# Kernel tuning notes

Measured on AMD Instinct MI355X. Metric: run time of the kernel, lower is better.

Reference implementation:

```python
import jax, jax.numpy as jnp
import numpy as np

H, W, P = 480, 600, 2048
N = H * W
_IU = np.triu_indices(4)

def _conv(x, w, b, stride=1):
    y = jax.lax.conv_general_dilated(x, w, (stride, stride), 'SAME',
                                     dimension_numbers=('NCHW', 'OIHW', 'NCHW'))
    return y + b[None, :, None, None]

def _gn(x, scale, bias, groups=16, eps=1e-5):
    n, c, h, w = x.shape
    xg = x.reshape(n, groups, c // groups, h, w)
    mu = xg.mean(axis=(2, 3, 4), keepdims=True)
    var = xg.var(axis=(2, 3, 4), keepdims=True)
    xg = (xg - mu) * jax.lax.rsqrt(var + eps)
    return xg.reshape(n, c, h, w) * scale[None, :, None, None] + bias[None, :, None, None]

def _lrelu(x):
    return jnp.where(x >= 0, x, 0.2 * x)

def setup_inputs():
    key = jax.random.key(0)
    ks = jax.random.split(key, 16)
    def he(k, shape, fan_in):
        return jax.random.normal(k, shape, jnp.float32) * np.float32(np.sqrt(2.0 / fan_in))
    return {
        'depth': jax.random.normal(ks[0], (1, 1, H, W), jnp.float32),
        'pose': jax.random.normal(ks[1], (P, 2, 8), jnp.float32),
        'target_mask': (jax.random.uniform(ks[2], (1, 1, H, W)) > 0.5).astype(jnp.float32),
        'pairs': jax.random.randint(ks[3], (P, 2), 0, N),
        'conv1_w': he(ks[4], (32, 3, 3, 3), 3 * 9), 'conv1_b': jnp.zeros(32),
        'gn1_s': jnp.ones(32), 'gn1_b': jnp.zeros(32),
        'conv2_w': he(ks[5], (64, 32, 3, 3), 32 * 9), 'conv2_b': jnp.zeros(64),
        'gn2_s': jnp.ones(64), 'gn2_b': jnp.zeros(64),
        'conv3_w': he(ks[6], (64, 64, 3, 3), 64 * 9), 'conv3_b': jnp.zeros(64),
        'gn3_s': jnp.ones(64), 'gn3_b': jnp.zeros(64),
        'conv4_w': he(ks[7], (64, 96, 3, 3), 96 * 9), 'conv4_b': jnp.zeros(64),
        'gn4_s': jnp.ones(64), 'gn4_b': jnp.zeros(64),
        'gate_w': he(ks[8], (15, 64), 15), 'gate_b': jnp.zeros(64),
        'hid_w': he(ks[9], (64, 64), 64), 'hid_b': jnp.zeros(64),
        'out_w': he(ks[10], (64, 1), 64), 'out_b': jnp.zeros(1),
    }

def _forward(depth, pose, target_mask, params, pairs):
    (c1w, c1b, g1s, g1b, c2w, c2b, g2s, g2b, c3w, c3b, g3s, g3b,
     c4w, c4b, g4s, g4b, gw, gb, hw_, hb, ow, ob) = params
    idx = pairs[:, 0]
    hh, ww = idx // W, idx % W
    # vectorized replacement of the per-pair python-loop scatter
    attn = jnp.zeros((1, 1, H, W), jnp.float32).at[0, 0, hh, ww].set(1.0)
    std_depth = (depth - depth.mean()) * 10.0
    x = jnp.concatenate([std_depth, target_mask, attn], axis=1)  # [1,3,H,W]
    # res_unet backbone (encoder-decoder, GroupNorm, leaky-relu 0.2)
    c1 = _lrelu(_gn(_conv(x, c1w, c1b), g1s, g1b))               # [1,32,H,W]
    d1 = _lrelu(_gn(_conv(c1, c2w, c2b, stride=2), g2s, g2b))    # [1,64,H/2,W/2]
    bm = _lrelu(_gn(_conv(d1, c3w, c3b), g3s, g3b))              # [1,64,H/2,W/2]
    up = jax.image.resize(bm, (1, 64, H, W), method='nearest')
    u = jnp.concatenate([up, c1], axis=1)                         # [1,96,H,W]
    feats = _lrelu(_gn(_conv(u, c4w, c4b), g4s, g4b))            # [1,64,H,W]
    # vectorized per-pair gather
    fg = feats.reshape(64, N)[:, idx].T                           # [P,64]
    fg = jnp.broadcast_to(fg[:, None, :], (P, 2, 64))
    dg = std_depth.reshape(N)[idx]
    dg = jnp.broadcast_to(dg[:, None, None], (P, 2, 1))
    quat = pose[:, :, :4]
    fingers = pose[:, :, 4:7]
    trans = pose[:, :, 7:8]
    outer = quat[..., :, None] * quat[..., None, :]               # sign-invariant q_i*q_j
    enc = outer[..., _IU[0], _IU[1]]                              # [P,2,10]
    cond = jnp.concatenate([enc, fingers, trans, dg], axis=-1)    # [P,2,15]
    # ContextGate_1d: gated attention over gathered features
    gate = jax.nn.sigmoid(cond @ gw + gb)                         # [P,2,64]
    h = fg * gate
    h = h * jax.lax.rsqrt(jnp.sum(h * h, axis=-1, keepdims=True) + 1e-8)
    h = _lrelu(h @ hw_ + hb)
    return jax.nn.silu(h) @ ow + ob                               # [P,2,1]

def reference(depth, pose, target_mask, pairs, conv1_w, conv1_b, gn1_s, gn1_b,
              conv2_w, conv2_b, gn2_s, gn2_b, conv3_w, conv3_b, gn3_s, gn3_b,
              conv4_w, conv4_b, gn4_s, gn4_b, gate_w, gate_b, hid_w, hid_b,
              out_w, out_b):
    params = (conv1_w, conv1_b, gn1_s, gn1_b, conv2_w, conv2_b, gn2_s, gn2_b,
              conv3_w, conv3_b, gn3_s, gn3_b, conv4_w, conv4_b, gn4_s, gn4_b,
              gate_w, gate_b, hid_w, hid_b, out_w, out_b)
    return _forward(depth, pose, target_mask, params, pairs)
```

## Files before the change

kernel.cpp:

```cpp
#include <hip/hip_runtime.h>
#include <math.h>

#define HH 480
#define WW 600
#define NN (HH*WW)
#define PP 2048
#define H2 240
#define W2 300
#define N2 (H2*W2)

typedef __bf16  bf16x8  __attribute__((ext_vector_type(8)));
typedef float   f32x4   __attribute__((ext_vector_type(4)));
typedef ushort  ushort8 __attribute__((ext_vector_type(8)));

__device__ __forceinline__ ushort f2b(float f) {
    unsigned u = __float_as_uint(f);
    unsigned r = (u + 0x7FFF + ((u >> 16) & 1)) >> 16;
    return (ushort)r;
}

constexpr size_t alup(size_t x) { return (x + 4095) & ~(size_t)4095; }
constexpr size_t OFF_X   = 4096;
constexpr size_t OFF_FT  = alup(OFF_X   + 3UL*NN*4);
constexpr size_t OFF_C1P = alup(OFF_FT  + 64UL*NN*4);
constexpr size_t OFF_D1R = alup(OFF_C1P + 32UL*NN*2);
constexpr size_t OFF_D1P = alup(OFF_D1R + 64UL*N2*4);
constexpr size_t OFF_BMP = alup(OFF_D1P + 64UL*N2*2);
constexpr size_t OFF_WB2 = alup(OFF_BMP + 64UL*N2*2);
constexpr size_t OFF_WB3 = alup(OFF_WB2 + 36864UL);
constexpr size_t OFF_WB4 = alup(OFF_WB3 + 73728UL);

__global__ void k_sum(const float* __restrict__ d, float* __restrict__ ws) {
    float s = 0.f;
    for (int i = blockIdx.x*blockDim.x + threadIdx.x; i < NN; i += gridDim.x*blockDim.x)
        s += d[i];
    #pragma unroll
    for (int o = 32; o; o >>= 1) s += __shfl_down(s, o, 64);
    __shared__ float sm[4];
    int wid = threadIdx.x >> 6;
    if ((threadIdx.x & 63) == 0) sm[wid] = s;
    __syncthreads();
    if (threadIdx.x == 0) {
        float t = 0.f;
        for (int w = 0; w < (int)(blockDim.x >> 6); ++w) t += sm[w];
        atomicAdd(ws, t);
    }
}

__global__ void k_buildx(const float* __restrict__ depth, const float* __restrict__ mask,
                         const float* __restrict__ ws, float* __restrict__ x) {
    int i = blockIdx.x*blockDim.x + threadIdx.x;
    if (i >= NN) return;
    float mean = ws[0] * (1.0f/NN);
    x[i]        = (depth[i] - mean) * 10.0f;
    x[NN + i]   = mask[i];
    x[2*NN + i] = 0.f;
}

__global__ void k_scatter(const int* __restrict__ pairs, float* __restrict__ x) {
    int p = blockIdx.x*blockDim.x + threadIdx.x;
    if (p < PP) x[2*NN + pairs[2*p]] = 1.0f;
}

__global__ void k_wcvt(const float* __restrict__ w, ushort* __restrict__ dst, int NCH) {
    int e = blockIdx.x*256 + threadIdx.x;
    int total = 9*NCH*64*32;
    if (e >= total) return;
    int k  = e & 31;
    int co = (e >> 5) & 63;
    int rest = e >> 11;
    int c = rest % NCH;
    int t = rest / NCH;
    dst[e] = f2b(w[(co*(NCH*32) + c*32 + k)*9 + t]);
}

template<int CIN, int TCO>
__global__ __launch_bounds__(64) void k_conv1(const float* __restrict__ in,
        const float* __restrict__ w, const float* __restrict__ bias,
        float* __restrict__ out) {
    int x   = blockIdx.x*64 + threadIdx.x;
    int y   = blockIdx.y;
    int co0 = blockIdx.z*TCO;
    if (x >= WW) return;
    float acc[TCO];
    #pragma unroll
    for (int c = 0; c < TCO; ++c) acc[c] = bias[co0+c];
    int  xb   = x - 1;
    bool xint = (xb >= 0) && (xb + 2 < WW);
    for (int ci = 0; ci < CIN; ++ci) {
        const float* ip = in + (long)ci*NN;
        float iv[3][3];
        #pragma unroll
        for (int dy = 0; dy < 3; ++dy) {
            int iy = y + dy - 1;
            if ((unsigned)iy < (unsigned)HH) {
                const float* rp = ip + (long)iy*WW + xb;
                if (xint) { iv[dy][0]=rp[0]; iv[dy][1]=rp[1]; iv[dy][2]=rp[2]; }
                else {
                    #pragma unroll
                    for (int dx = 0; dx < 3; ++dx) {
                        int ix = xb + dx;
                        iv[dy][dx] = ((unsigned)ix < (unsigned)WW) ? ip[(long)iy*WW+ix] : 0.f;
                    }
                }
            } else iv[dy][0]=iv[dy][1]=iv[dy][2]=0.f;
        }
        const float* wp = w + ((long)co0*CIN + ci)*9;
        #pragma unroll
        for (int c = 0; c < TCO; ++c)
            #pragma unroll
            for (int k = 0; k < 9; ++k)
                acc[c] += iv[k/3][k%3] * wp[(long)c*CIN*9 + k];
    }
    float* op = out + (size_t)(y*WW + x)*32 + co0;
    #pragma unroll
    for (int c = 0; c < TCO; ++c) op[c] = acc[c];
}

__global__ __launch_bounds__(256) void k_gnstats_pk(const float* __restrict__ x,
        float* __restrict__ stat, int npx) {
    int o = threadIdx.x & 3;
    float s[8], s2[8];
    #pragma unroll
    for (int j = 0; j < 8; ++j) { s[j] = 0.f; s2[j] = 0.f; }
    for (int e = blockIdx.x*256 + threadIdx.x; e < npx*4; e += gridDim.x*256) {
        int px = e >> 2;
        const float* p = x + (size_t)px*32 + o*8;
        #pragma unroll
        for (int j = 0; j < 8; ++j) { float v = p[j]; s[j] += v; s2[j] += v*v; }
    }
    float gs[4], gs2[4];
    #pragma unroll
    for (int j = 0; j < 4; ++j) { gs[j] = s[2*j]+s[2*j+1]; gs2[j] = s2[2*j]+s2[2*j+1]; }
    #pragma unroll
    for (int off = 4; off < 64; off <<= 1)
        #pragma unroll
        for (int j = 0; j < 4; ++j) {
            gs[j]  += __shfl_xor(gs[j],  off, 64);
            gs2[j] += __shfl_xor(gs2[j], off, 64);
        }
    __shared__ float sm[4][4][8];
    int wv = threadIdx.x >> 6;
    if ((threadIdx.x & 63) < 4) {
        #pragma unroll
        for (int j = 0; j < 4; ++j) { sm[wv][o][j] = gs[j]; sm[wv][o][4+j] = gs2[j]; }
    }
    __syncthreads();
    if (threadIdx.x < 32) {
        int o2 = threadIdx.x >> 3, k = threadIdx.x & 7;
        float t = sm[0][o2][k] + sm[1][o2][k] + sm[2][o2][k] + sm[3][o2][k];
        int g = o2*4 + (k & 3);
        atomicAdd(&stat[(k >> 2)*16 + g], t);
    }
}

template<int CH, int CHPER>
__global__ void k_gnpack(const float* __restrict__ x, ushort* __restrict__ y,
                         const float* __restrict__ scale, const float* __restrict__ bias,
                         const float* __restrict__ stat, int npx) {
    constexpr int PARTS = CH/16;
    int e = blockIdx.x*256 + threadIdx.x;
    if (e >= npx*PARTS) return;
    int px   = e / PARTS;
    int part = e - px*PARTS;
    const float* p = x + (size_t)px*CH + part*16;
    ushort*      q = y + (size_t)px*CH + part*16;
    float cnt = (float)CHPER * (float)npx;
    #pragma unroll
    for (int j = 0; j < 16; ++j) {
        int c = part*16 + j;
        int g = c / CHPER;
        float mu  = stat[g] / cnt;
        float var = stat[16+g] / cnt - mu*mu;
        float rs  = rsqrtf(var + 1e-5f);
        float v = (p[j] - mu) * rs * scale[c] + bias[c];
        q[j] = f2b(v >= 0.f ? v : 0.2f*v);
    }
}

template<int MODE>
__global__ __launch_bounds__(256) void k_sconv(const ushort* __restrict__ inA,
        const ushort* __restrict__ inB, const ushort* __restrict__ wb,
        const float* __restrict__ bias, float* __restrict__ out,
        float* __restrict__ stat) {
    constexpr int Wo   = (MODE==4) ? WW : W2;
    constexpr int NCH  = (MODE==2) ? 1 : (MODE==3) ? 2 : 3;
    constexpr int NPT  = (MODE==2) ? 2 : 4;
    constexpr int ROWS = (MODE==2) ? 9 : 6;
    constexpr int PXS  = 68;
    constexpr int CPITCH = 36;
    constexpr int UNITS = ROWS*PXS*4;
    constexpr int Hi = (MODE==3) ? H2 : HH;
    constexpr int Wi = (MODE==3) ? W2 : WW;
    __shared__ __align__(16) ushort sh[ROWS*PXS*CPITCH];
    __shared__ float sred[4][16][2];

    int w    = threadIdx.x >> 6;
    int lane = threadIdx.x & 63;
    int lm   = lane & 15;
    int lg   = lane >> 4;
    int y0   = blockIdx.y*4;
    int x0   = blockIdx.x*(NPT*16);
    int y    = y0 + w;
    int iy0  = (MODE==2) ? 2*y0 : y0 - 1;
    int ix0  = (MODE==2) ? 2*x0 : x0 - 1;

    f32x4 acc[4][NPT];
    #pragma unroll
    for (int ct = 0; ct < 4; ++ct)
        #pragma unroll
        for (int pt = 0; pt < NPT; ++pt) acc[ct][pt] = 0.f;

    int dsbase = (((MODE==2 ? 2*w*PXS + 2*lm : w*PXS + lm))*CPITCH + lg*8);

    #pragma unroll
    for (int kc = 0; kc < NCH; ++kc) {
        if (kc) __syncthreads();
        #pragma unroll
        for (int u0 = 0; u0 < UNITS; u0 += 256) {
            int u = u0 + threadIdx.x;
            if (u < UNITS) {
                int r  = u / (PXS*4);
                int rm = u - r*(PXS*4);
                int px = rm >> 2;
                int q  = rm & 3;
                int iy = iy0 + r;
                int ix = ix0 + px;
                ushort8 val = {};
                if ((unsigned)iy < (unsigned)Hi && (unsigned)ix < (unsigned)Wi) {
                    const ushort* sp;
                    if (MODE==2)      sp = inA + ((size_t)iy*WW + ix)*32 + q*8;
                    else if (MODE==3) sp = inA + ((size_t)iy*W2 + ix)*64 + kc*32 + q*8;
                    else if (kc < 2)  sp = inA + ((size_t)(iy>>1)*W2 + (ix>>1))*64 + kc*32 + q*8;
                    else              sp = inB + ((size_t)iy*WW + ix)*32 + q*8;
                    val = *(const ushort8*)sp;
                }
                *(ushort8*)&sh[(r*PXS + px)*CPITCH + q*8] = val;
            }
        }
        __syncthreads();
        #pragma unroll
        for (int t = 0; t < 9; ++t) {
            const int dy = t/3, dx = t - 3*(t/3);
            const ushort* wp = wb + (size_t)((t*NCH + kc)*64)*32;
            bf16x8 a[4];
            #pragma unroll
            for (int ct = 0; ct < 4; ++ct)
                a[ct] = *(const bf16x8*)(wp + (ct*16 + lm)*32 + lg*8);
            #pragma unroll
            for (int pt = 0; pt < NPT; ++pt) {
                int off = (dy*PXS + (MODE==2 ? pt*32 + dx : pt*16 + dx))*CPITCH;
                bf16x8 b = *(const bf16x8*)&sh[dsbase + off];
                #pragma unroll
                for (int ct = 0; ct < 4; ++ct)
                    acc[ct][pt] = __builtin_amdgcn_mfma_f32_16x16x32_bf16(a[ct], b, acc[ct][pt], 0, 0, 0);
            }
        }
    }

    #pragma unroll
    for (int ct = 0; ct < 4; ++ct) {
        float s = 0.f, s2 = 0.f;
        #pragma unroll
        for (int pt = 0; pt < NPT; ++pt) {
            int pxg = x0 + pt*16 + lm;
            bool vld = pxg < Wo;
            f32x4 r;
            #pragma unroll
            for (int reg = 0; reg < 4; ++reg) {
                int co = ct*16 + lg*4 + reg;
                float v = acc[ct][pt][reg] + bias[co];
                r[reg] = v;
                if (vld) { s += v; s2 += v*v; }
            }
            if (vld)
                *(f32x4*)(out + (size_t)(y*Wo + pxg)*64 + ct*16 + lg*4) = r;
        }
        #pragma unroll
        for (int o = 1; o < 16; o <<= 1) {
            s  += __shfl_xor(s,  o, 64);
            s2 += __shfl_xor(s2, o, 64);
        }
        if (lm == 0) { sred[w][ct*4+lg][0] = s; sred[w][ct*4+lg][1] = s2; }
    }
    __syncthreads();
    if (threadIdx.x < 32) {
        int g = threadIdx.x >> 1, k = threadIdx.x & 1;
        float t = sred[0][g][k] + sred[1][g][k] + sred[2][g][k] + sred[3][g][k];
        atomicAdd(&stat[k*16 + g], t);
    }
}

__global__ void k_mlp(const float* __restrict__ pose, const float* __restrict__ sd,
                      const int* __restrict__ pairs, const float* __restrict__ feats,
                      const float* __restrict__ g4s, const float* __restrict__ g4b,
                      const float* __restrict__ st4,
                      const float* __restrict__ gw, const float* __restrict__ gb,
                      const float* __restrict__ hw, const float* __restrict__ hb,
                      const float* __restrict__ ow, const float* __restrict__ ob,
                      float* __restrict__ out) {
    int wid  = threadIdx.x >> 6;
    int lane = threadIdx.x & 63;
    int t = blockIdx.x*4 + wid;
    int p = t >> 1;
    const float* pp = pose + t*8;
    float q0=pp[0], q1=pp[1], q2=pp[2], q3=pp[3];
    float f0=pp[4], f1=pp[5], f2=pp[6], tr=pp[7];
    int idx = pairs[2*p];
    float dg = sd[idx];
    float cond[15] = {q0*q0,q0*q1,q0*q2,q0*q3,q1*q1,q1*q2,q1*q3,q2*q2,q2*q3,q3*q3,
                      f0,f1,f2,tr,dg};
    float acc = gb[lane];
    #pragma unroll
    for (int k = 0; k < 15; ++k) acc += cond[k]*gw[k*64+lane];
    float gate = 1.f/(1.f+expf(-acc));
    float raw = feats[(size_t)idx*64 + lane];
    int   g4  = lane >> 2;
    float cnt = 4.0f * (float)NN;
    float mu  = st4[g4] / cnt;
    float var = st4[16+g4] / cnt - mu*mu;
    float rs  = rsqrtf(var + 1e-5f);
    float fv  = (raw - mu) * rs * g4s[lane] + g4b[lane];
    float fg  = fv >= 0.f ? fv : 0.2f*fv;
    float h = fg*gate;
    float ss = h*h;
    #pragma unroll
    for (int o = 32; o; o >>= 1) ss += __shfl_xor(ss, o, 64);
    h *= rsqrtf(ss + 1e-8f);
    __shared__ float hs[4][64];
    hs[wid][lane] = h;
    __syncthreads();
    float a2 = hb[lane];
    #pragma unroll 8
    for (int d = 0; d < 64; ++d) a2 += hs[wid][d]*hw[d*64+lane];
    float h2 = a2 >= 0.f ? a2 : 0.2f*a2;
    float si = h2 / (1.f+expf(-h2));
    float v = si * ow[lane];
    #pragma unroll
    for (int o = 32; o; o >>= 1) v += __shfl_xor(v, o, 64);
    if (lane == 0) out[t] = v + ob[0];
}

extern "C" void kernel_launch(void* const* d_in, const int* in_sizes, int n_in,
                              void* d_out, int out_size, void* d_ws, size_t ws_size,
                              hipStream_t stream) {
    const float* depth = (const float*)d_in[0];
    const float* pose  = (const float*)d_in[1];
    const float* mask  = (const float*)d_in[2];
    const int*   pairs = (const int*)  d_in[3];
    const float* c1w = (const float*)d_in[4];  const float* c1b = (const float*)d_in[5];
    const float* g1s = (const float*)d_in[6];  const float* g1b = (const float*)d_in[7];
    const float* c2w = (const float*)d_in[8];  const float* c2b = (const float*)d_in[9];
    const float* g2s = (const float*)d_in[10]; const float* g2b = (const float*)d_in[11];
    const float* c3w = (const float*)d_in[12]; const float* c3b = (const float*)d_in[13];
    const float* g3s = (const float*)d_in[14]; const float* g3b = (const float*)d_in[15];
    const float* c4w = (const float*)d_in[16]; const float* c4b = (const float*)d_in[17];
    const float* g4s = (const float*)d_in[18]; const float* g4b = (const float*)d_in[19];
    const float* gw  = (const float*)d_in[20]; const float* gb  = (const float*)d_in[21];
    const float* hw_ = (const float*)d_in[22]; const float* hb  = (const float*)d_in[23];
    const float* ow  = (const float*)d_in[24]; const float* ob  = (const float*)d_in[25];

    char* base = (char*)d_ws;
    float*  stats = (float*) base;
    float*  X   = (float*) (base + OFF_X);
    float*  FT  = (float*) (base + OFF_FT);
    float*  C1R = FT;
    ushort* C1P = (ushort*)(base + OFF_C1P);
    float*  D1R = (float*) (base + OFF_D1R);
    ushort* D1P = (ushort*)(base + OFF_D1P);
    ushort* BMP = (ushort*)(base + OFF_BMP);
    ushort* WB2 = (ushort*)(base + OFF_WB2);
    ushort* WB3 = (ushort*)(base + OFF_WB3);
    ushort* WB4 = (ushort*)(base + OFF_WB4);
    float* st1 = stats + 16;
    float* st2 = stats + 64;
    float* st3 = stats + 112;
    float* st4 = stats + 160;

    hipMemsetAsync(d_ws, 0, 1024, stream);

    k_sum    <<<1024, 256, 0, stream>>>(depth, stats);
    k_buildx <<<(NN+255)/256, 256, 0, stream>>>(depth, mask, stats, X);
    k_scatter<<<(PP+255)/256, 256, 0, stream>>>(pairs, X);
    k_wcvt   <<< 72, 256, 0, stream>>>(c2w, WB2, 1);
    k_wcvt   <<<144, 256, 0, stream>>>(c3w, WB3, 2);
    k_wcvt   <<<216, 256, 0, stream>>>(c4w, WB4, 3);

    k_conv1<3,16><<<dim3(10, HH, 2), 64, 0, stream>>>(X, c1w, c1b, C1R);
    k_gnstats_pk<<<256, 256, 0, stream>>>(C1R, st1, NN);
    k_gnpack<32,2><<<(NN*2+255)/256, 256, 0, stream>>>(C1R, C1P, g1s, g1b, st1, NN);

    k_sconv<2><<<dim3(10, 60), 256, 0, stream>>>(C1P, nullptr, WB2, c2b, D1R, st2);
    k_gnpack<64,4><<<(N2*4+255)/256, 256, 0, stream>>>(D1R, D1P, g2s, g2b, st2, N2);

    k_sconv<3><<<dim3(5, 60), 256, 0, stream>>>(D1P, nullptr, WB3, c3b, D1R, st3);
    k_gnpack<64,4><<<(N2*4+255)/256, 256, 0, stream>>>(D1R, BMP, g3s, g3b, st3, N2);

    k_sconv<4><<<dim3(10, 120), 256, 0, stream>>>(BMP, C1P, WB4, c4b, FT, st4);

    k_mlp<<<(2*PP)/4, 256, 0, stream>>>(pose, X, pairs, FT, g4s, g4b, st4,
                                        gw, gb, hw_, hb, ow, ob, (float*)d_out);
}
```

Measured before the change: 322.5 us.

## Fuse GroupNorm into conv loads, emit stats from conv1, compact final features

Conv1 now writes bf16 output and reduces its GroupNorm statistics in-kernel, which removes the separate stats and pack passes. Each sconv applies the preceding GroupNorm and LeakyReLU while staging its input tile into shared memory, so intermediate activations are stored raw in bf16 instead of fp32 and then repacked. The last conv writes only the pixels referenced by pairs into a compact buffer through a slot map, avoiding a full 64-channel fp32 feature map write. In exchange, normalisation work is repeated on halo loads, and an extra memset and slot-map kernel are added.

```diff
diff --git a/kernel.cpp b/kernel.cpp
--- a/kernel.cpp
+++ b/kernel.cpp
@@ -18,17 +18,20 @@
     unsigned r = (u + 0x7FFF + ((u >> 16) & 1)) >> 16;
     return (ushort)r;
 }
+__device__ __forceinline__ float b2f(ushort u) {
+    return __uint_as_float(((unsigned)u) << 16);
+}
 
 constexpr size_t alup(size_t x) { return (x + 4095) & ~(size_t)4095; }
-constexpr size_t OFF_X   = 4096;
-constexpr size_t OFF_FT  = alup(OFF_X   + 3UL*NN*4);
-constexpr size_t OFF_C1P = alup(OFF_FT  + 64UL*NN*4);
-constexpr size_t OFF_D1R = alup(OFF_C1P + 32UL*NN*2);
-constexpr size_t OFF_D1P = alup(OFF_D1R + 64UL*N2*4);
-constexpr size_t OFF_BMP = alup(OFF_D1P + 64UL*N2*2);
-constexpr size_t OFF_WB2 = alup(OFF_BMP + 64UL*N2*2);
-constexpr size_t OFF_WB3 = alup(OFF_WB2 + 36864UL);
-constexpr size_t OFF_WB4 = alup(OFF_WB3 + 73728UL);
+constexpr size_t OFF_X    = 4096;
+constexpr size_t OFF_C1R  = alup(OFF_X   + 3UL*NN*4);
+constexpr size_t OFF_RW2  = alup(OFF_C1R + 32UL*NN*2);
+constexpr size_t OFF_RW3  = alup(OFF_RW2 + 64UL*N2*2);
+constexpr size_t OFF_WB2  = alup(OFF_RW3 + 64UL*N2*2);
+constexpr size_t OFF_WB3  = alup(OFF_WB2 + 36864UL);
+constexpr size_t OFF_WB4  = alup(OFF_WB3 + 73728UL);
+constexpr size_t OFF_SLOT = alup(OFF_WB4 + 110592UL);
+constexpr size_t OFF_CMP  = alup(OFF_SLOT + (size_t)NN*4);
 
 __global__ void k_sum(const float* __restrict__ d, float* __restrict__ ws) {
     float s = 0.f;
@@ -60,6 +63,11 @@
 __global__ void k_scatter(const int* __restrict__ pairs, float* __restrict__ x) {
     int p = blockIdx.x*blockDim.x + threadIdx.x;
     if (p < PP) x[2*NN + pairs[2*p]] = 1.0f;
+}
+
+__global__ void k_slot(const int* __restrict__ pairs, int* __restrict__ slotmap) {
+    int p = blockIdx.x*blockDim.x + threadIdx.x;
+    if (p < PP) slotmap[pairs[2*p]] = p;
 }
 
 __global__ void k_wcvt(const float* __restrict__ w, ushort* __restrict__ dst, int NCH) {
@@ -77,111 +85,81 @@
 template<int CIN, int TCO>
 __global__ __launch_bounds__(64) void k_conv1(const float* __restrict__ in,
         const float* __restrict__ w, const float* __restrict__ bias,
-        float* __restrict__ out) {
+        ushort* __restrict__ outb, float* __restrict__ stat) {
     int x   = blockIdx.x*64 + threadIdx.x;
     int y   = blockIdx.y;
     int co0 = blockIdx.z*TCO;
-    if (x >= WW) return;
+    bool valid = x < WW;
     float acc[TCO];
     #pragma unroll
     for (int c = 0; c < TCO; ++c) acc[c] = bias[co0+c];
-    int  xb   = x - 1;
-    bool xint = (xb >= 0) && (xb + 2 < WW);
-    for (int ci = 0; ci < CIN; ++ci) {
-        const float* ip = in + (long)ci*NN;
-        float iv[3][3];
-        #pragma unroll
-        for (int dy = 0; dy < 3; ++dy) {
-            int iy = y + dy - 1;
-            if ((unsigned)iy < (unsigned)HH) {
-                const float* rp = ip + (long)iy*WW + xb;
-                if (xint) { iv[dy][0]=rp[0]; iv[dy][1]=rp[1]; iv[dy][2]=rp[2]; }
-                else {
-                    #pragma unroll
-                    for (int dx = 0; dx < 3; ++dx) {
-                        int ix = xb + dx;
-                        iv[dy][dx] = ((unsigned)ix < (unsigned)WW) ? ip[(long)iy*WW+ix] : 0.f;
+    if (valid) {
+        int  xb   = x - 1;
+        bool xint = (xb >= 0) && (xb + 2 < WW);
+        for (int ci = 0; ci < CIN; ++ci) {
+            const float* ip = in + (long)ci*NN;
+            float iv[3][3];
+            #pragma unroll
+            for (int dy = 0; dy < 3; ++dy) {
+                int iy = y + dy - 1;
+                if ((unsigned)iy < (unsigned)HH) {
+                    const float* rp = ip + (long)iy*WW + xb;
+                    if (xint) { iv[dy][0]=rp[0]; iv[dy][1]=rp[1]; iv[dy][2]=rp[2]; }
+                    else {
+                        #pragma unroll
+                        for (int dx = 0; dx < 3; ++dx) {
+                            int ix = xb + dx;
+                            iv[dy][dx] = ((unsigned)ix < (unsigned)WW) ? ip[(long)iy*WW+ix] : 0.f;
+                        }
                     }
-                }
-            } else iv[dy][0]=iv[dy][1]=iv[dy][2]=0.f;
-        }
-        const float* wp = w + ((long)co0*CIN + ci)*9;
-        #pragma unroll
-        for (int c = 0; c < TCO; ++c)
-            #pragma unroll
-            for (int k = 0; k < 9; ++k)
-                acc[c] += iv[k/3][k%3] * wp[(long)c*CIN*9 + k];
-    }
-    float* op = out + (size_t)(y*WW + x)*32 + co0;
-    #pragma unroll
-    for (int c = 0; c < TCO; ++c) op[c] = acc[c];
-}
-
-__global__ __launch_bounds__(256) void k_gnstats_pk(const float* __restrict__ x,
-        float* __restrict__ stat, int npx) {
-    int o = threadIdx.x & 3;
-    float s[8], s2[8];
-    #pragma unroll
-    for (int j = 0; j < 8; ++j) { s[j] = 0.f; s2[j] = 0.f; }
-    for (int e = blockIdx.x*256 + threadIdx.x; e < npx*4; e += gridDim.x*256) {
-        int px = e >> 2;
-        const float* p = x + (size_t)px*32 + o*8;
-        #pragma unroll
-        for (int j = 0; j < 8; ++j) { float v = p[j]; s[j] += v; s2[j] += v*v; }
-    }
-    float gs[4], gs2[4];
-    #pragma unroll
-    for (int j = 0; j < 4; ++j) { gs[j] = s[2*j]+s[2*j+1]; gs2[j] = s2[2*j]+s2[2*j+1]; }
-    #pragma unroll
-    for (int off = 4; off < 64; off <<= 1)
-        #pragma unroll
-        for (int j = 0; j < 4; ++j) {
-            gs[j]  += __shfl_xor(gs[j],  off, 64);
-            gs2[j] += __shfl_xor(gs2[j], off, 64);
-        }
-    __shared__ float sm[4][4][8];
-    int wv = threadIdx.x >> 6;
-    if ((threadIdx.x & 63) < 4) {
-        #pragma unroll
-        for (int j = 0; j < 4; ++j) { sm[wv][o][j] = gs[j]; sm[wv][o][4+j] = gs2[j]; }
-    }
-    __syncthreads();
-    if (threadIdx.x < 32) {
-        int o2 = threadIdx.x >> 3, k = threadIdx.x & 7;
-        float t = sm[0][o2][k] + sm[1][o2][k] + sm[2][o2][k] + sm[3][o2][k];
-        int g = o2*4 + (k & 3);
-        atomicAdd(&stat[(k >> 2)*16 + g], t);
-    }
-}
-
-template<int CH, int CHPER>
-__global__ void k_gnpack(const float* __restrict__ x, ushort* __restrict__ y,
-                         const float* __restrict__ scale, const float* __restrict__ bias,
-                         const float* __restrict__ stat, int npx) {
-    constexpr int PARTS = CH/16;
-    int e = blockIdx.x*256 + threadIdx.x;
-    if (e >= npx*PARTS) return;
-    int px   = e / PARTS;
-    int part = e - px*PARTS;
-    const float* p = x + (size_t)px*CH + part*16;
-    ushort*      q = y + (size_t)px*CH + part*16;
-    float cnt = (float)CHPER * (float)npx;
-    #pragma unroll
-    for (int j = 0; j < 16; ++j) {
-        int c = part*16 + j;
-        int g = c / CHPER;
-        float mu  = stat[g] / cnt;
-        float var = stat[16+g] / cnt - mu*mu;
-        float rs  = rsqrtf(var + 1e-5f);
-        float v = (p[j] - mu) * rs * scale[c] + bias[c];
-        q[j] = f2b(v >= 0.f ? v : 0.2f*v);
+                } else iv[dy][0]=iv[dy][1]=iv[dy][2]=0.f;
+            }
+            const float* wp = w + ((long)co0*CIN + ci)*9;
+            #pragma unroll
+            for (int c = 0; c < TCO; ++c)
+                #pragma unroll
+                for (int k = 0; k < 9; ++k)
+                    acc[c] += iv[k/3][k%3] * wp[(long)c*CIN*9 + k];
+        }
+        ushort8 p0, p1;
+        #pragma unroll
+        for (int j = 0; j < 8; ++j) { p0[j] = f2b(acc[j]); p1[j] = f2b(acc[8+j]); }
+        ushort* op = outb + (size_t)(y*WW + x)*32 + co0;
+        *(ushort8*)op     = p0;
+        *(ushort8*)(op+8) = p1;
+    }
+    float s[TCO/2], s2[TCO/2];
+    #pragma unroll
+    for (int j = 0; j < TCO/2; ++j) {
+        float a = valid ? acc[2*j]   : 0.f;
+        float b = valid ? acc[2*j+1] : 0.f;
+        s[j] = a + b; s2[j] = a*a + b*b;
+    }
+    #pragma unroll
+    for (int o = 1; o < 64; o <<= 1)
+        #pragma unroll
+        for (int j = 0; j < TCO/2; ++j) {
+            s[j]  += __shfl_xor(s[j],  o, 64);
+            s2[j] += __shfl_xor(s2[j], o, 64);
+        }
+    if (threadIdx.x == 0) {
+        #pragma unroll
+        for (int j = 0; j < TCO/2; ++j) {
+            int g = (co0 >> 1) + j;
+            atomicAdd(&stat[g],    s[j]);
+            atomicAdd(&stat[16+g], s2[j]);
+        }
     }
 }
 
 template<int MODE>
-__global__ __launch_bounds__(256) void k_sconv(const ushort* __restrict__ inA,
-        const ushort* __restrict__ inB, const ushort* __restrict__ wb,
-        const float* __restrict__ bias, float* __restrict__ out,
+__global__ __launch_bounds__(256) void k_sconv(
+        const ushort* __restrict__ inA, const ushort* __restrict__ inB,
+        const ushort* __restrict__ wb, const float* __restrict__ bias,
+        const float* __restrict__ gsA, const float* __restrict__ gbA, const float* __restrict__ stA,
+        const float* __restrict__ gsB, const float* __restrict__ gbB, const float* __restrict__ stB,
+        ushort* __restrict__ outb,
+        const int* __restrict__ slotmap, float* __restrict__ compact,
         float* __restrict__ stat) {
     constexpr int Wo   = (MODE==4) ? WW : W2;
     constexpr int NCH  = (MODE==2) ? 1 : (MODE==3) ? 2 : 3;
@@ -199,6 +177,7 @@
     int lane = threadIdx.x & 63;
     int lm   = lane & 15;
     int lg   = lane >> 4;
+    int q    = threadIdx.x & 3;
     int y0   = blockIdx.y*4;
     int x0   = blockIdx.x*(NPT*16);
     int y    = y0 + w;
@@ -216,6 +195,25 @@
     #pragma unroll
     for (int kc = 0; kc < NCH; ++kc) {
         if (kc) __syncthreads();
+        float Ac[8], Bc[8];
+        {
+            const bool useB = (MODE==4) && (kc == 2);
+            const float* gs = useB ? gsB : gsA;
+            const float* gb = useB ? gbB : gbA;
+            const float* st = useB ? stB : stA;
+            const float cnt = (MODE==2 || useB) ? 2.0f*(float)NN : 4.0f*(float)N2;
+            const int   shp = (MODE==2 || useB) ? 1 : 2;
+            const int   cb  = (MODE==2 || useB) ? q*8 : kc*32 + q*8;
+            #pragma unroll
+            for (int j = 0; j < 8; ++j) {
+                int c = cb + j, g = c >> shp;
+                float mu  = st[g] / cnt;
+                float var = st[16+g] / cnt - mu*mu;
+                float rs  = rsqrtf(var + 1e-5f);
+                float a   = rs * gs[c];
+                Ac[j] = a; Bc[j] = gb[c] - mu*a;
+            }
+        }
         #pragma unroll
         for (int u0 = 0; u0 < UNITS; u0 += 256) {
             int u = u0 + threadIdx.x;
@@ -223,19 +221,23 @@
                 int r  = u / (PXS*4);
                 int rm = u - r*(PXS*4);
                 int px = rm >> 2;
-                int q  = rm & 3;
                 int iy = iy0 + r;
                 int ix = ix0 + px;
-                ushort8 val = {};
+                ushort8 pk = {};
                 if ((unsigned)iy < (unsigned)Hi && (unsigned)ix < (unsigned)Wi) {
                     const ushort* sp;
                     if (MODE==2)      sp = inA + ((size_t)iy*WW + ix)*32 + q*8;
                     else if (MODE==3) sp = inA + ((size_t)iy*W2 + ix)*64 + kc*32 + q*8;
                     else if (kc < 2)  sp = inA + ((size_t)(iy>>1)*W2 + (ix>>1))*64 + kc*32 + q*8;
                     else              sp = inB + ((size_t)iy*WW + ix)*32 + q*8;
-                    val = *(const ushort8*)sp;
+                    ushort8 raw = *(const ushort8*)sp;
+                    #pragma unroll
+                    for (int j = 0; j < 8; ++j) {
+                        float t = b2f(raw[j])*Ac[j] + Bc[j];
+                        pk[j] = f2b(t >= 0.f ? t : 0.2f*t);
+                    }
                 }
-                *(ushort8*)&sh[(r*PXS + px)*CPITCH + q*8] = val;
+                *(ushort8*)&sh[(r*PXS + px)*CPITCH + q*8] = pk;
             }
         }
         __syncthreads();
@@ -258,30 +260,64 @@
         }
     }
 
-    #pragma unroll
-    for (int ct = 0; ct < 4; ++ct) {
-        float s = 0.f, s2 = 0.f;
-        #pragma unroll
-        for (int pt = 0; pt < NPT; ++pt) {
+    if (MODE != 4) {
+        #pragma unroll
+        for (int ct = 0; ct < 4; ++ct) {
+            float s = 0.f, s2 = 0.f;
+            #pragma unroll
+            for (int pt = 0; pt < NPT; ++pt) {
+                int pxg = x0 + pt*16 + lm;
+                bool vld = pxg < Wo;
+                ushort4 pk;
+                #pragma unroll
+                for (int reg = 0; reg < 4; ++reg) {
+                    int co = ct*16 + lg*4 + reg;
+                    float v = acc[ct][pt][reg] + bias[co];
+                    ((ushort*)&pk)[reg] = f2b(v);
+                    if (vld) { s += v; s2 += v*v; }
+                }
+                if (vld)
+                    *(ushort4*)(outb + (size_t)(y*Wo + pxg)*64 + ct*16 + lg*4) = pk;
+            }
+            #pragma unroll
+            for (int o = 1; o < 16; o <<= 1) {
+                s  += __shfl_xor(s,  o, 64);
+                s2 += __shfl_xor(s2, o, 64);
+            }
+            if (lm == 0) { sred[w][ct*4+lg][0] = s; sred[w][ct*4+lg][1] = s2; }
+        }
+    } else {
+        int slots[4];
+        #pragma unroll
+        for (int pt = 0; pt < 4; ++pt) {
             int pxg = x0 + pt*16 + lm;
-            bool vld = pxg < Wo;
-            f32x4 r;
-            #pragma unroll
-            for (int reg = 0; reg < 4; ++reg) {
-                int co = ct*16 + lg*4 + reg;
-                float v = acc[ct][pt][reg] + bias[co];
-                r[reg] = v;
-                if (vld) { s += v; s2 += v*v; }
-            }
-            if (vld)
-                *(f32x4*)(out + (size_t)(y*Wo + pxg)*64 + ct*16 + lg*4) = r;
-        }
-        #pragma unroll
-        for (int o = 1; o < 16; o <<= 1) {
-            s  += __shfl_xor(s,  o, 64);
-            s2 += __shfl_xor(s2, o, 64);
-        }
-        if (lm == 0) { sred[w][ct*4+lg][0] = s; sred[w][ct*4+lg][1] = s2; }
+            slots[pt] = (pxg < Wo) ? slotmap[(size_t)y*Wo + pxg] : -1;
+        }
+        #pragma unroll
+        for (int ct = 0; ct < 4; ++ct) {
+            float s = 0.f, s2 = 0.f;
+            #pragma unroll
+            for (int pt = 0; pt < 4; ++pt) {
+                int pxg = x0 + pt*16 + lm;
+                bool vld = pxg < Wo;
+                f32x4 r;
+                #pragma unroll
+                for (int reg = 0; reg < 4; ++reg) {
+                    int co = ct*16 + lg*4 + reg;
+                    float v = acc[ct][pt][reg] + bias[co];
+                    r[reg] = v;
+                    if (vld) { s += v; s2 += v*v; }
+                }
+                if (slots[pt] >= 0)
+                    *(f32x4*)(compact + (size_t)slots[pt]*64 + ct*16 + lg*4) = r;
+            }
+            #pragma unroll
+            for (int o = 1; o < 16; o <<= 1) {
+                s  += __shfl_xor(s,  o, 64);
+                s2 += __shfl_xor(s2, o, 64);
+            }
+            if (lm == 0) { sred[w][ct*4+lg][0] = s; sred[w][ct*4+lg][1] = s2; }
+        }
     }
     __syncthreads();
     if (threadIdx.x < 32) {
@@ -292,7 +328,8 @@
 }
 
 __global__ void k_mlp(const float* __restrict__ pose, const float* __restrict__ sd,
-                      const int* __restrict__ pairs, const float* __restrict__ feats,
+                      const int* __restrict__ pairs, const int* __restrict__ slotmap,
+                      const float* __restrict__ compact,
                       const float* __restrict__ g4s, const float* __restrict__ g4b,
                       const float* __restrict__ st4,
                       const float* __restrict__ gw, const float* __restrict__ gb,
@@ -314,7 +351,8 @@
     #pragma unroll
     for (int k = 0; k < 15; ++k) acc += cond[k]*gw[k*64+lane];
     float gate = 1.f/(1.f+expf(-acc));
-    float raw = feats[(size_t)idx*64 + lane];
+    int slot = slotmap[idx];
+    float raw = compact[(size_t)slot*64 + lane];
     int   g4  = lane >> 2;
     float cnt = 4.0f * (float)NN;
     float mu  = st4[g4] / cnt;
@@ -362,42 +400,42 @@
 
     char* base = (char*)d_ws;
     float*  stats = (float*) base;
-    float*  X   = (float*) (base + OFF_X);
-    float*  FT  = (float*) (base + OFF_FT);
-    float*  C1R = FT;
-    ushort* C1P = (ushort*)(base + OFF_C1P);
-    float*  D1R = (float*) (base + OFF_D1R);
-    ushort* D1P = (ushort*)(base + OFF_D1P);
-    ushort* BMP = (ushort*)(base + OFF_BMP);
-    ushort* WB2 = (ushort*)(base + OFF_WB2);
-    ushort* WB3 = (ushort*)(base + OFF_WB3);
-    ushort* WB4 = (ushort*)(base + OFF_WB4);
+    float*  X    = (float*) (base + OFF_X);
+    ushort* C1R  = (ushort*)(base + OFF_C1R);
+    ushort* RW2  = (ushort*)(base + OFF_RW2);
+    ushort* RW3  = (ushort*)(base + OFF_RW3);
+    ushort* WB2  = (ushort*)(base + OFF_WB2);
+    ushort* WB3  = (ushort*)(base + OFF_WB3);
+    ushort* WB4  = (ushort*)(base + OFF_WB4);
+    int*    SLOT = (int*)   (base + OFF_SLOT);
+    float*  CMP  = (float*) (base + OFF_CMP);
     float* st1 = stats + 16;
     float* st2 = stats + 64;
     float* st3 = stats + 112;
     float* st4 = stats + 160;
 
     hipMemsetAsync(d_ws, 0, 1024, stream);
+    hipMemsetAsync(SLOT, 0xFF, (size_t)NN*4, stream);
 
     k_sum    <<<1024, 256, 0, stream>>>(depth, stats);
     k_buildx <<<(NN+255)/256, 256, 0, stream>>>(depth, mask, stats, X);
     k_scatter<<<(PP+255)/256, 256, 0, stream>>>(pairs, X);
+    k_slot   <<<(PP+255)/256, 256, 0, stream>>>(pairs, SLOT);
     k_wcvt   <<< 72, 256, 0, stream>>>(c2w, WB2, 1);
     k_wcvt   <<<144, 256, 0, stream>>>(c3w, WB3, 2);
     k_wcvt   <<<216, 256, 0, stream>>>(c4w, WB4, 3);
 
-    k_conv1<3,16><<<dim3(10, HH, 2), 64, 0, stream>>>(X, c1w, c1b, C1R);
-    k_gnstats_pk<<<256, 256, 0, stream>>>(C1R, st1, NN);
-    k_gnpack<32,2><<<(NN*2+255)/256, 256, 0, stream>>>(C1R, C1P, g1s, g1b, st1, NN);
-
-    k_sconv<2><<<dim3(10, 60), 256, 0, stream>>>(C1P, nullptr, WB2, c2b, D1R, st2);
-    k_gnpack<64,4><<<(N2*4+255)/256, 256, 0, stream>>>(D1R, D1P, g2s, g2b, st2, N2);
-
-    k_sconv<3><<<dim3(5, 60), 256, 0, stream>>>(D1P, nullptr, WB3, c3b, D1R, st3);
-    k_gnpack<64,4><<<(N2*4+255)/256, 256, 0, stream>>>(D1R, BMP, g3s, g3b, st3, N2);
-
-    k_sconv<4><<<dim3(10, 120), 256, 0, stream>>>(BMP, C1P, WB4, c4b, FT, st4);
-
-    k_mlp<<<(2*PP)/4, 256, 0, stream>>>(pose, X, pairs, FT, g4s, g4b, st4,
+    k_conv1<3,16><<<dim3(10, HH, 2), 64, 0, stream>>>(X, c1w, c1b, C1R, st1);
+
+    k_sconv<2><<<dim3(10, 60), 256, 0, stream>>>(C1R, nullptr, WB2, c2b,
+        g1s, g1b, st1, nullptr, nullptr, nullptr, RW2, nullptr, nullptr, st2);
+
+    k_sconv<3><<<dim3(5, 60), 256, 0, stream>>>(RW2, nullptr, WB3, c3b,
+        g2s, g2b, st2, nullptr, nullptr, nullptr, RW3, nullptr, nullptr, st3);
+
+    k_sconv<4><<<dim3(10, 120), 256, 0, stream>>>(RW3, C1R, WB4, c4b,
+        g3s, g3b, st3, g1s, g1b, st1, nullptr, SLOT, CMP, st4);
+
+    k_mlp<<<(2*PP)/4, 256, 0, stream>>>(pose, X, pairs, SLOT, CMP, g4s, g4b, st4,
                                         gw, gb, hw_, hb, ow, ob, (float*)d_out);
 }
```

After: 1.281 ms. +297.3%, slower.
